# Performance work log

Measured on AMD Instinct MI355X. Metric: run time of the kernel, lower is better.

The kernel has to match this reference:

```python
import jax, jax.numpy as jnp
import numpy as np

D_MODEL, D_STATE, D_CONV, EXPAND = 1024, 16, 4, 2
D_INNER = EXPAND * D_MODEL  # 2048
DT_RANK = (D_MODEL + 15) // 16  # 64
BATCH, SEQ = 2, 2048


def setup_inputs() -> dict:
    key = jax.random.key(0)
    ks = jax.random.split(key, 8)
    s = 0.02
    A = jnp.tile(jnp.arange(1, D_STATE + 1, dtype=jnp.float32), (D_INNER, 1))
    return {
        "x": jax.random.normal(ks[0], (BATCH, SEQ, D_MODEL), jnp.float32),
        "in_proj_w": jax.random.normal(ks[1], (D_MODEL, 2 * D_INNER), jnp.float32) * s,
        "conv_w": jax.random.normal(ks[2], (D_INNER, 1, D_CONV), jnp.float32) * s,
        "conv_b": jnp.zeros((D_INNER,), jnp.float32),
        "x_proj_w": jax.random.normal(ks[3], (D_INNER, DT_RANK + 2 * D_STATE), jnp.float32) * s,
        "dt_proj_w": jax.random.normal(ks[4], (DT_RANK, D_INNER), jnp.float32) * s,
        "dt_proj_b": jnp.zeros((D_INNER,), jnp.float32),
        "A_log": jnp.log(A),
        "D": jnp.ones((D_INNER,), jnp.float32),
        "out_proj_w": jax.random.normal(ks[5], (D_INNER, D_MODEL), jnp.float32) * s,
    }


def _mamba(x, in_proj_w, conv_w, conv_b, x_proj_w, dt_proj_w, dt_proj_b, A_log, D, out_proj_w):
    d_inner, d_state = A_log.shape
    dt_rank = dt_proj_w.shape[0]
    seq_len = x.shape[1]

    xr = x @ in_proj_w                       # (B, L, 2*ED)
    xb, res = jnp.split(xr, 2, axis=-1)      # each (B, L, ED)

    # causal depthwise conv1d (torch pads both sides then truncates to seq_len
    # == left-pad-only causal conv)
    xc = jnp.swapaxes(xb, 1, 2)              # (B, ED, L)
    xc = jax.lax.conv_general_dilated(
        xc, conv_w, window_strides=(1,),
        padding=[(conv_w.shape[-1] - 1, 0)],
        dimension_numbers=("NCH", "OIH", "NCH"),
        feature_group_count=d_inner)
    xc = xc + conv_b[None, :, None]
    u = jax.nn.silu(jnp.swapaxes(xc, 1, 2))  # (B, L, ED)

    dbc = u @ x_proj_w                       # (B, L, dt_rank + 2*N)
    dt, Bc, Cc = jnp.split(dbc, [dt_rank, dt_rank + d_state], axis=-1)
    dt = jax.nn.softplus(dt @ dt_proj_w + dt_proj_b)  # (B, L, ED)
    A = -jnp.exp(A_log)                      # (ED, N)

    def step(h, xs):
        dt_i, B_i, C_i, u_i = xs             # (B,ED), (B,N), (B,N), (B,ED)
        dA = jnp.exp(dt_i[:, :, None] * A)   # (B, ED, N)
        h = h * dA + (dt_i * u_i)[:, :, None] * B_i[:, None, :]
        y = jnp.einsum("bdn,bn->bd", h, C_i) + D * u_i
        return h, y

    h0 = jnp.zeros((x.shape[0], d_inner, d_state), x.dtype)
    xs = (jnp.swapaxes(dt, 0, 1), jnp.swapaxes(Bc, 0, 1),
          jnp.swapaxes(Cc, 0, 1), jnp.swapaxes(u, 0, 1))
    _, ys = jax.lax.scan(step, h0, xs)       # ys: (L, B, ED)
    y_ssm = jnp.swapaxes(ys, 0, 1)           # (B, L, ED)

    y = y_ssm * jax.nn.silu(res)
    return y @ out_proj_w                    # (B, L, d_model)


def reference(x, in_proj_w, conv_w, conv_b, x_proj_w, dt_proj_w, dt_proj_b, A_log, D, out_proj_w):
    return _mamba(x, in_proj_w, conv_w, conv_b, x_proj_w, dt_proj_w, dt_proj_b, A_log, D, out_proj_w)
```

## Files before the change

### kernel.cpp

```cpp
#include <hip/hip_runtime.h>
#include <cstddef>
#include <cstdint>

#define BATCH 2
#define SEQ   2048
#define DM    1024
#define ED    2048
#define NS    16
#define DR    64
#define NROWS (BATCH*SEQ)

#define NCHUNK 32
#define CLEN   64
#define CSTATES (BATCH*ED*NS)

#define OFF_XB    ((size_t)0)
#define OFF_RESH  ((size_t)8388608)
#define OFF_U     ((size_t)12582912)
#define OFF_DT    ((size_t)20971520)
#define OFF_DBC   ((size_t)29360128)
#define OFF_PART  ((size_t)29753344)

typedef _Float16 half8 __attribute__((ext_vector_type(8)));
typedef _Float16 half4 __attribute__((ext_vector_type(4)));
typedef float    floatx4 __attribute__((ext_vector_type(4)));

__device__ __forceinline__ float silu_f(float x) { return x / (1.f + __expf(-x)); }

__device__ __forceinline__ void gload_lds16(const _Float16* g, _Float16* l) {
  __builtin_amdgcn_global_load_lds(
      (const __attribute__((address_space(1))) void*)g,
      (__attribute__((address_space(3))) void*)l, 16, 0, 0);
}

template<int BN, int WGM, int WGN, int EPI, int KSPLIT>
__global__ __launch_bounds__(256)
void hgemm(const _Float16* __restrict__ A, int lda,
           const _Float16* __restrict__ Bt, int ldb,
           float* __restrict__ C, _Float16* __restrict__ Ch,
           size_t cslice, int N, int K) {
  constexpr int BM = 128;
  constexpr int FM = BM / 16 / WGM;
  constexpr int FN = BN / 16 / WGN;
  __shared__ _Float16 sA[BM * 32];
  __shared__ _Float16 sB[BN * 32];
  const int tid = threadIdx.x;
  const int ln  = tid & 63;
  const int wid = tid >> 6;
  const int wm  = wid % WGM;
  const int wn  = wid / WGM;
  const int m0  = blockIdx.y * BM;
  const int n0  = blockIdx.x * BN;
  const int l15 = ln & 15;
  const int q   = ln >> 4;

  const int kLen = K / KSPLIT;
  const int kbeg = blockIdx.z * kLen;
  if (KSPLIT > 1) C += (size_t)blockIdx.z * cslice;

  floatx4 acc[FM][FN];
  #pragma unroll
  for (int i = 0; i < FM; ++i)
    #pragma unroll
    for (int j = 0; j < FN; ++j)
      acc[i][j] = floatx4{0.f, 0.f, 0.f, 0.f};

  for (int k0 = kbeg; k0 < kbeg + kLen; k0 += 32) {
    __syncthreads();
    #pragma unroll
    for (int s = 0; s < (BM * 4 + 255) / 256; ++s) {
      const int i = s * 256 + tid;
      if (BM * 4 % 256 == 0 || i < BM * 4) {
        const int m = i >> 2;
        const int cg = (i & 3) ^ ((m >> 1) & 3);
        gload_lds16(A + (size_t)(m0 + m) * lda + k0 + cg * 8, sA + i * 8);
      }
    }
    #pragma unroll
    for (int s = 0; s < (BN * 4 + 255) / 256; ++s) {
      const int i = s * 256 + tid;
      if (BN * 4 % 256 == 0 || i < BN * 4) {
        const int n = i >> 2;
        const int cg = (i & 3) ^ ((n >> 1) & 3);
        gload_lds16(Bt + (size_t)(n0 + n) * ldb + k0 + cg * 8, sB + i * 8);
      }
    }
    __syncthreads();

    half8 af[FM], bf[FN];
    #pragma unroll
    for (int fm = 0; fm < FM; ++fm) {
      const int mr = wm * FM * 16 + fm * 16 + l15;
      const int cl = q ^ ((mr >> 1) & 3);
      af[fm] = *(const half8*)(sA + mr * 32 + cl * 8);
    }
    #pragma unroll
    for (int fn = 0; fn < FN; ++fn) {
      const int nr = wn * FN * 16 + fn * 16 + l15;
      const int cl = q ^ ((nr >> 1) & 3);
      bf[fn] = *(const half8*)(sB + nr * 32 + cl * 8);
    }
    #pragma unroll
    for (int fm = 0; fm < FM; ++fm)
      #pragma unroll
      for (int fn = 0; fn < FN; ++fn)
        acc[fm][fn] = __builtin_amdgcn_mfma_f32_16x16x32_f16(
            af[fm], bf[fn], acc[fm][fn], 0, 0, 0);
  }

  #pragma unroll
  for (int fm = 0; fm < FM; ++fm) {
    #pragma unroll
    for (int fn = 0; fn < FN; ++fn) {
      const int col = n0 + wn * FN * 16 + fn * 16 + l15;
      #pragma unroll
      for (int r = 0; r < 4; ++r) {
        const int row = m0 + wm * FM * 16 + fm * 16 + q * 4 + r;
        const float v = acc[fm][fn][r];
        if (EPI == 2) {
          if (col < ED) C[(size_t)row * ED + col] = v;
          else          Ch[(size_t)row * ED + (col - ED)] = (_Float16)silu_f(v);
        } else {
          C[(size_t)row * N + col] = v;
        }
      }
    }
  }
}

__global__ __launch_bounds__(256)
void cvt_half_kernel(const float* __restrict__ src, _Float16* __restrict__ dst) {
  const int i = (blockIdx.x * 256 + threadIdx.x) * 4;
  const float4 v = *(const float4*)(src + i);
  half4 o;
  o[0] = (_Float16)v.x; o[1] = (_Float16)v.y;
  o[2] = (_Float16)v.z; o[3] = (_Float16)v.w;
  *(half4*)(dst + i) = o;
}

__global__ __launch_bounds__(256)
void transpose_h_kernel(const float* __restrict__ src, _Float16* __restrict__ dst,
                        int R, int C) {
  __shared__ float t[32][33];
  const int tx = threadIdx.x & 31, ty = threadIdx.x >> 5;
  const int c0 = blockIdx.x * 32, r0 = blockIdx.y * 32;
  #pragma unroll
  for (int s = 0; s < 4; ++s)
    t[ty + s * 8][tx] = src[(size_t)(r0 + ty + s * 8) * C + c0 + tx];
  __syncthreads();
  #pragma unroll
  for (int s = 0; s < 4; ++s)
    dst[(size_t)(c0 + ty + s * 8) * R + r0 + tx] = (_Float16)t[tx][ty + s * 8];
}

template<int EPI>
__global__ __launch_bounds__(256)
void sgemm128(const float* __restrict__ A, int lda,
              const float* __restrict__ Bm, const float* __restrict__ bias,
              float* __restrict__ C, int N, int K) {
  __shared__ float As[8][128];
  __shared__ float Bs[8][128];
  const int tid  = threadIdx.x;
  const int m0   = blockIdx.y * 128;
  const int n0   = blockIdx.x * 128;
  const int tx   = tid & 15;
  const int ty   = tid >> 4;
  const int arow = tid >> 1;
  const int acol = (tid & 1) * 4;
  const int brow = tid >> 5;
  const int bcol = (tid & 31) * 4;

  const float* Ap = A + (size_t)(m0 + arow) * lda + acol;
  const float* Bp = Bm + (size_t)brow * N + n0 + bcol;

  float acc[8][8];
  #pragma unroll
  for (int i = 0; i < 8; ++i)
    #pragma unroll
    for (int j = 0; j < 8; ++j) acc[i][j] = 0.f;

  for (int k0 = 0; k0 < K; k0 += 8) {
    const float4 av = *(const float4*)(Ap + k0);
    const float4 bv = *(const float4*)(Bp + (size_t)k0 * N);
    __syncthreads();
    As[acol + 0][arow] = av.x;
    As[acol + 1][arow] = av.y;
    As[acol + 2][arow] = av.z;
    As[acol + 3][arow] = av.w;
    *(float4*)&Bs[brow][bcol] = bv;
    __syncthreads();
    #pragma unroll
    for (int k = 0; k < 8; ++k) {
      float a[8], b[8];
      *(float4*)(a)     = *(const float4*)&As[k][ty * 8];
      *(float4*)(a + 4) = *(const float4*)&As[k][ty * 8 + 4];
      *(float4*)(b)     = *(const float4*)&Bs[k][tx * 8];
      *(float4*)(b + 4) = *(const float4*)&Bs[k][tx * 8 + 4];
      #pragma unroll
      for (int i = 0; i < 8; ++i)
        #pragma unroll
        for (int j = 0; j < 8; ++j)
          acc[i][j] = fmaf(a[i], b[j], acc[i][j]);
    }
  }

  #pragma unroll
  for (int i = 0; i < 8; ++i) {
    float* Cp = C + (size_t)(m0 + ty * 8 + i) * N + n0 + tx * 8;
    #pragma unroll
    for (int j = 0; j < 8; ++j) {
      float v = acc[i][j];
      if (EPI == 1) {
        v += bias[n0 + tx * 8 + j];
        v = fmaxf(v, 0.f) + log1pf(__expf(-fabsf(v)));
      }
      Cp[j] = v;
    }
  }
}

__global__ __launch_bounds__(256)
void conv_silu_kernel(const float* __restrict__ xb, const float* __restrict__ w,
                      const float* __restrict__ cb, float* __restrict__ u,
                      _Float16* __restrict__ u_h) {
  const int idx = blockIdx.x * 256 + threadIdx.x;
  const int d = idx & (ED - 1);
  const int t = (idx >> 11) & (SEQ - 1);
  const float4 wv = ((const float4*)w)[d];
  const float* base = xb + (size_t)(idx >> 11) * ED + d;
  float acc = cb[d];
  acc = fmaf(wv.w, base[0], acc);
  if (t >= 1) acc = fmaf(wv.z, base[-ED], acc);
  if (t >= 2) acc = fmaf(wv.y, base[-2 * ED], acc);
  if (t >= 3) acc = fmaf(wv.x, base[-3 * ED], acc);
  const float v = silu_f(acc);
  u[idx] = v;
  u_h[idx] = (_Float16)v;
}

__global__ __launch_bounds__(256)
void xproj_reduce(const float* __restrict__ part, float* __restrict__ dbc) {
  const int idx = blockIdx.x * 256 + threadIdx.x;
  float s = 0.f;
  #pragma unroll
  for (int r = 0; r < 8; ++r) s += part[(size_t)r * NROWS * 96 + idx];
  dbc[idx] = s;
}

__global__ __launch_bounds__(256)
void scan2_summary(const float* __restrict__ dt, const float* __restrict__ u,
                   const float* __restrict__ dbc, const float* __restrict__ A_log,
                   float* __restrict__ Pbuf, float* __restrict__ Sbuf) {
  const int d = blockIdx.x * 256 + threadIdx.x;
  const int b = blockIdx.y;
  const int g = blockIdx.z;

  float Adn[16];
  {
    const float4* al = (const float4*)(A_log + (size_t)d * NS);
    #pragma unroll
    for (int i = 0; i < 4; ++i) {
      const float4 v = al[i];
      Adn[i * 4 + 0] = -__expf(v.x); Adn[i * 4 + 1] = -__expf(v.y);
      Adn[i * 4 + 2] = -__expf(v.z); Adn[i * 4 + 3] = -__expf(v.w);
    }
  }
  float P[16], S[16];
  #pragma unroll
  for (int n = 0; n < 16; ++n) { P[n] = 1.f; S[n] = 0.f; }

  const size_t row0 = (size_t)b * SEQ + (size_t)g * CLEN;
  const float* dtp = dt + row0 * ED + d;
  const float* up  = u  + row0 * ED + d;

  for (int t = 0; t < CLEN; ++t) {
    const float dti = dtp[(size_t)t * ED];
    const float ui  = up[(size_t)t * ED];
    const float4* bc = (const float4*)(dbc + (row0 + t) * 96 + DR);
    float Bv[16];
    #pragma unroll
    for (int i = 0; i < 4; ++i) {
      const float4 v = bc[i];
      Bv[i * 4 + 0] = v.x; Bv[i * 4 + 1] = v.y;
      Bv[i * 4 + 2] = v.z; Bv[i * 4 + 3] = v.w;
    }
    const float dtu = dti * ui;
    #pragma unroll
    for (int n = 0; n < 16; ++n) {
      const float a = __expf(dti * Adn[n]);
      S[n] = fmaf(S[n], a, dtu * Bv[n]);
      P[n] *= a;
    }
  }
  const size_t c0 = (size_t)g * CSTATES + ((size_t)(b * ED + d)) * NS;
  #pragma unroll
  for (int i = 0; i < 4; ++i) {
    *(float4*)(Pbuf + c0 + i * 4) = float4{P[i*4], P[i*4+1], P[i*4+2], P[i*4+3]};
    *(float4*)(Sbuf + c0 + i * 4) = float4{S[i*4], S[i*4+1], S[i*4+2], S[i*4+3]};
  }
}

__global__ __launch_bounds__(256)
void scan2_compose(float* __restrict__ Pbuf, const float* __restrict__ Sbuf) {
  const unsigned c = blockIdx.x * 256 + threadIdx.x;
  float h = 0.f;
  for (int g = 0; g < NCHUNK; ++g) {
    const size_t idx = (size_t)g * CSTATES + c;
    const float p = Pbuf[idx], s = Sbuf[idx];
    Pbuf[idx] = h;
    h = fmaf(p, h, s);
  }
}

__global__ __launch_bounds__(256)
void scan2_apply(const float* __restrict__ dt, const float* __restrict__ u,
                 const float* __restrict__ dbc, const float* __restrict__ A_log,
                 const float* __restrict__ Dp, const float* __restrict__ Pbuf,
                 _Float16* __restrict__ resh) {
  const int d = blockIdx.x * 256 + threadIdx.x;
  const int b = blockIdx.y;
  const int g = blockIdx.z;

  float Adn[16];
  {
    const float4* al = (const float4*)(A_log + (size_t)d * NS);
    #pragma unroll
    for (int i = 0; i < 4; ++i) {
      const float4 v = al[i];
      Adn[i * 4 + 0] = -__expf(v.x); Adn[i * 4 + 1] = -__expf(v.y);
      Adn[i * 4 + 2] = -__expf(v.z); Adn[i * 4 + 3] = -__expf(v.w);
    }
  }
  const float Dd = Dp[d];
  float h[16];
  const size_t c0 = (size_t)g * CSTATES + ((size_t)(b * ED + d)) * NS;
  #pragma unroll
  for (int i = 0; i < 4; ++i) {
    const float4 v = *(const float4*)(Pbuf + c0 + i * 4);
    h[i * 4 + 0] = v.x; h[i * 4 + 1] = v.y;
    h[i * 4 + 2] = v.z; h[i * 4 + 3] = v.w;
  }

  const size_t row0 = (size_t)b * SEQ + (size_t)g * CLEN;
  const float* dtp = dt + row0 * ED + d;
  const float* up  = u  + row0 * ED + d;
  _Float16* rp = resh + row0 * ED + d;

  for (int t = 0; t < CLEN; ++t) {
    const float dti = dtp[(size_t)t * ED];
    const float ui  = up[(size_t)t * ED];
    const float4* bc = (const float4*)(dbc + (row0 + t) * 96 + DR);
    float Bv[16], Cv[16];
    #pragma unroll
    for (int i = 0; i < 4; ++i) {
      const float4 v = bc[i];
      Bv[i * 4 + 0] = v.x; Bv[i * 4 + 1] = v.y;
      Bv[i * 4 + 2] = v.z; Bv[i * 4 + 3] = v.w;
      const float4 w = bc[4 + i];
      Cv[i * 4 + 0] = w.x; Cv[i * 4 + 1] = w.y;
      Cv[i * 4 + 2] = w.z; Cv[i * 4 + 3] = w.w;
    }
    const float dtu = dti * ui;
    float y = Dd * ui;
    #pragma unroll
    for (int n = 0; n < 16; ++n) {
      const float a = __expf(dti * Adn[n]);
      h[n] = fmaf(h[n], a, dtu * Bv[n]);
      y = fmaf(h[n], Cv[n], y);
    }
    const float sres = (float)rp[(size_t)t * ED];
    rp[(size_t)t * ED] = (_Float16)(y * sres);
  }
}

extern "C" void kernel_launch(void* const* d_in, const int* in_sizes, int n_in,
                              void* d_out, int out_size, void* d_ws, size_t ws_size,
                              hipStream_t stream) {
  (void)in_sizes; (void)n_in; (void)out_size; (void)ws_size;
  const float* x     = (const float*)d_in[0];
  const float* Win   = (const float*)d_in[1];
  const float* convw = (const float*)d_in[2];
  const float* convb = (const float*)d_in[3];
  const float* Wx    = (const float*)d_in[4];
  const float* Wdt   = (const float*)d_in[5];
  const float* bdt   = (const float*)d_in[6];
  const float* Alog  = (const float*)d_in[7];
  const float* Dp    = (const float*)d_in[8];
  const float* Wout  = (const float*)d_in[9];

  float* ws   = (float*)d_ws;
  float* xb   = ws + OFF_XB;
  _Float16* resh = (_Float16*)(ws + OFF_RESH);
  float* u    = ws + OFF_U;
  float* dt   = ws + OFF_DT;
  float* dbc  = ws + OFF_DBC;
  float* part = ws + OFF_PART;
  float* Pbuf = part;
  float* Sbuf = part + (size_t)NCHUNK * CSTATES;
  _Float16* Woutt = (_Float16*)(part + 4194304);
  _Float16* Wxt   = (_Float16*)(part + 5242880);
  float* out  = (float*)d_out;

  _Float16* x_h  = (_Float16*)(ws + OFF_DT);
  _Float16* Wint = (_Float16*)(ws + OFF_DT + 2097152);
  _Float16* u_h  = (_Float16*)(ws + OFF_DT + 4194304);

  cvt_half_kernel<<<(NROWS * DM) / 1024, 256, 0, stream>>>(x, x_h);
  transpose_h_kernel<<<dim3((2 * ED) / 32, DM / 32), 256, 0, stream>>>(
      Win, Wint, DM, 2 * ED);
  transpose_h_kernel<<<dim3(96 / 32, ED / 32), 256, 0, stream>>>(
      Wx, Wxt, ED, 96);
  transpose_h_kernel<<<dim3(DM / 32, ED / 32), 256, 0, stream>>>(
      Wout, Woutt, ED, DM);
  hgemm<128, 2, 2, 2, 1><<<dim3((2 * ED) / 128, NROWS / 128), 256, 0, stream>>>(
      x_h, DM, Wint, DM, xb, resh, 0, 2 * ED, DM);
  conv_silu_kernel<<<(NROWS * ED) / 256, 256, 0, stream>>>(xb, convw, convb, u, u_h);
  hgemm<96, 4, 1, 0, 8><<<dim3(1, NROWS / 128, 8), 256, 0, stream>>>(
      u_h, ED, Wxt, ED, part, nullptr, (size_t)NROWS * 96, 96, ED);
  xproj_reduce<<<(NROWS * 96) / 256, 256, 0, stream>>>(part, dbc);
  sgemm128<1><<<dim3(ED / 128, NROWS / 128), 256, 0, stream>>>(
      dbc, 96, Wdt, bdt, dt, ED, DR);
  scan2_summary<<<dim3(ED / 256, BATCH, NCHUNK), 256, 0, stream>>>(
      dt, u, dbc, Alog, Pbuf, Sbuf);
  scan2_compose<<<CSTATES / 256, 256, 0, stream>>>(Pbuf, Sbuf);
  scan2_apply<<<dim3(ED / 256, BATCH, NCHUNK), 256, 0, stream>>>(
      dt, u, dbc, Alog, Dp, Pbuf, resh);
  hgemm<64, 4, 1, 0, 1><<<dim3(DM / 64, NROWS / 128), 256, 0, stream>>>(
      resh, ED, Woutt, ED, out, nullptr, 0, DM, ED);
}
```

Measured before the change: 374.6 us.

## Fuse prep kernels, recompute conv in scan, move dt_proj to fp16 MFMA

Merges the input cast and the three weight transposes, plus a new Wdt transpose, into one prep kernel to cut launch count. The scan kernels now recompute the causal conv and SiLU from xb instead of reading a stored fp32 u buffer, which removes that write and reread. dt_proj moves from the fp32 SIMT sgemm to the fp16 MFMA hgemm with a fused bias+softplus epilogue. The scan chunking goes from 32 chunks of 64 to 64 chunks of 32, giving more parallelism but more compose work, and the half-precision dt input adds rounding error.

Result: faster. 364.5 us (-2.7%).

```diff
diff --git a/kernel.cpp b/kernel.cpp
--- a/kernel.cpp
+++ b/kernel.cpp
@@ -10,13 +10,13 @@
 #define DR    64
 #define NROWS (BATCH*SEQ)
 
-#define NCHUNK 32
-#define CLEN   64
+#define NCHUNK 64
+#define CLEN   32
 #define CSTATES (BATCH*ED*NS)
 
 #define OFF_XB    ((size_t)0)
 #define OFF_RESH  ((size_t)8388608)
-#define OFF_U     ((size_t)12582912)
+#define OFF_PS    ((size_t)12582912)
 #define OFF_DT    ((size_t)20971520)
 #define OFF_DBC   ((size_t)29360128)
 #define OFF_PART  ((size_t)29753344)
@@ -37,6 +37,7 @@
 __global__ __launch_bounds__(256)
 void hgemm(const _Float16* __restrict__ A, int lda,
            const _Float16* __restrict__ Bt, int ldb,
+           const float* __restrict__ bias,
            float* __restrict__ C, _Float16* __restrict__ Ch,
            size_t cslice, int N, int K) {
   constexpr int BM = 128;
@@ -116,10 +117,14 @@
       #pragma unroll
       for (int r = 0; r < 4; ++r) {
         const int row = m0 + wm * FM * 16 + fm * 16 + q * 4 + r;
-        const float v = acc[fm][fn][r];
+        float v = acc[fm][fn][r];
         if (EPI == 2) {
           if (col < ED) C[(size_t)row * ED + col] = v;
           else          Ch[(size_t)row * ED + (col - ED)] = (_Float16)silu_f(v);
+        } else if (EPI == 3) {
+          v += bias[col];
+          v = fmaxf(v, 0.f) + log1pf(__expf(-fabsf(v)));
+          C[(size_t)row * N + col] = v;
         } else {
           C[(size_t)row * N + col] = v;
         }
@@ -128,22 +133,13 @@
   }
 }
 
-__global__ __launch_bounds__(256)
-void cvt_half_kernel(const float* __restrict__ src, _Float16* __restrict__ dst) {
-  const int i = (blockIdx.x * 256 + threadIdx.x) * 4;
-  const float4 v = *(const float4*)(src + i);
-  half4 o;
-  o[0] = (_Float16)v.x; o[1] = (_Float16)v.y;
-  o[2] = (_Float16)v.z; o[3] = (_Float16)v.w;
-  *(half4*)(dst + i) = o;
-}
-
-__global__ __launch_bounds__(256)
-void transpose_h_kernel(const float* __restrict__ src, _Float16* __restrict__ dst,
-                        int R, int C) {
+__device__ __forceinline__ void transpose_tile(const float* __restrict__ src,
+                                               _Float16* __restrict__ dst,
+                                               int R, int C, int bx, int by,
+                                               int tid) {
   __shared__ float t[32][33];
-  const int tx = threadIdx.x & 31, ty = threadIdx.x >> 5;
-  const int c0 = blockIdx.x * 32, r0 = blockIdx.y * 32;
+  const int tx = tid & 31, ty = tid >> 5;
+  const int c0 = bx * 32, r0 = by * 32;
   #pragma unroll
   for (int s = 0; s < 4; ++s)
     t[ty + s * 8][tx] = src[(size_t)(r0 + ty + s * 8) * C + c0 + tx];
@@ -153,76 +149,39 @@
     dst[(size_t)(c0 + ty + s * 8) * R + r0 + tx] = (_Float16)t[tx][ty + s * 8];
 }
 
-template<int EPI>
-__global__ __launch_bounds__(256)
-void sgemm128(const float* __restrict__ A, int lda,
-              const float* __restrict__ Bm, const float* __restrict__ bias,
-              float* __restrict__ C, int N, int K) {
-  __shared__ float As[8][128];
-  __shared__ float Bs[8][128];
-  const int tid  = threadIdx.x;
-  const int m0   = blockIdx.y * 128;
-  const int n0   = blockIdx.x * 128;
-  const int tx   = tid & 15;
-  const int ty   = tid >> 4;
-  const int arow = tid >> 1;
-  const int acol = (tid & 1) * 4;
-  const int brow = tid >> 5;
-  const int bcol = (tid & 31) * 4;
-
-  const float* Ap = A + (size_t)(m0 + arow) * lda + acol;
-  const float* Bp = Bm + (size_t)brow * N + n0 + bcol;
-
-  float acc[8][8];
-  #pragma unroll
-  for (int i = 0; i < 8; ++i)
-    #pragma unroll
-    for (int j = 0; j < 8; ++j) acc[i][j] = 0.f;
-
-  for (int k0 = 0; k0 < K; k0 += 8) {
-    const float4 av = *(const float4*)(Ap + k0);
-    const float4 bv = *(const float4*)(Bp + (size_t)k0 * N);
-    __syncthreads();
-    As[acol + 0][arow] = av.x;
-    As[acol + 1][arow] = av.y;
-    As[acol + 2][arow] = av.z;
-    As[acol + 3][arow] = av.w;
-    *(float4*)&Bs[brow][bcol] = bv;
-    __syncthreads();
-    #pragma unroll
-    for (int k = 0; k < 8; ++k) {
-      float a[8], b[8];
-      *(float4*)(a)     = *(const float4*)&As[k][ty * 8];
-      *(float4*)(a + 4) = *(const float4*)&As[k][ty * 8 + 4];
-      *(float4*)(b)     = *(const float4*)&Bs[k][tx * 8];
-      *(float4*)(b + 4) = *(const float4*)&Bs[k][tx * 8 + 4];
-      #pragma unroll
-      for (int i = 0; i < 8; ++i)
-        #pragma unroll
-        for (int j = 0; j < 8; ++j)
-          acc[i][j] = fmaf(a[i], b[j], acc[i][j]);
-    }
-  }
-
-  #pragma unroll
-  for (int i = 0; i < 8; ++i) {
-    float* Cp = C + (size_t)(m0 + ty * 8 + i) * N + n0 + tx * 8;
-    #pragma unroll
-    for (int j = 0; j < 8; ++j) {
-      float v = acc[i][j];
-      if (EPI == 1) {
-        v += bias[n0 + tx * 8 + j];
-        v = fmaxf(v, 0.f) + log1pf(__expf(-fabsf(v)));
-      }
-      Cp[j] = v;
-    }
+#define PREP_BLOCKS 10560
+__global__ __launch_bounds__(256)
+void prep_kernel(const float* __restrict__ x, _Float16* __restrict__ x_h,
+                 const float* __restrict__ Win, _Float16* __restrict__ Wint,
+                 const float* __restrict__ Wout, _Float16* __restrict__ Woutt,
+                 const float* __restrict__ Wx, _Float16* __restrict__ Wxt,
+                 const float* __restrict__ Wdt, _Float16* __restrict__ Wdtt) {
+  const int bid = blockIdx.x, tid = threadIdx.x;
+  if (bid < 4096) {
+    const int i = bid * 1024 + tid * 4;
+    const float4 v = *(const float4*)(x + i);
+    half4 o;
+    o[0] = (_Float16)v.x; o[1] = (_Float16)v.y;
+    o[2] = (_Float16)v.z; o[3] = (_Float16)v.w;
+    *(half4*)(x_h + i) = o;
+  } else if (bid < 8192) {
+    const int t = bid - 4096;
+    transpose_tile(Win, Wint, DM, 2 * ED, t & 127, t >> 7, tid);
+  } else if (bid < 10240) {
+    const int t = bid - 8192;
+    transpose_tile(Wout, Woutt, ED, DM, t & 31, t >> 5, tid);
+  } else if (bid < 10432) {
+    const int t = bid - 10240;
+    transpose_tile(Wx, Wxt, ED, 96, t % 3, t / 3, tid);
+  } else {
+    const int t = bid - 10432;
+    transpose_tile(Wdt, Wdtt, DR, ED, t & 63, t >> 6, tid);
   }
 }
 
 __global__ __launch_bounds__(256)
 void conv_silu_kernel(const float* __restrict__ xb, const float* __restrict__ w,
-                      const float* __restrict__ cb, float* __restrict__ u,
-                      _Float16* __restrict__ u_h) {
+                      const float* __restrict__ cb, _Float16* __restrict__ u_h) {
   const int idx = blockIdx.x * 256 + threadIdx.x;
   const int d = idx & (ED - 1);
   const int t = (idx >> 11) & (SEQ - 1);
@@ -233,22 +192,31 @@
   if (t >= 1) acc = fmaf(wv.z, base[-ED], acc);
   if (t >= 2) acc = fmaf(wv.y, base[-2 * ED], acc);
   if (t >= 3) acc = fmaf(wv.x, base[-3 * ED], acc);
-  const float v = silu_f(acc);
-  u[idx] = v;
-  u_h[idx] = (_Float16)v;
-}
-
-__global__ __launch_bounds__(256)
-void xproj_reduce(const float* __restrict__ part, float* __restrict__ dbc) {
+  u_h[idx] = (_Float16)silu_f(acc);
+}
+
+__global__ __launch_bounds__(256)
+void xproj_reduce(const float* __restrict__ part, float* __restrict__ dbc,
+                  _Float16* __restrict__ dbc64h) {
   const int idx = blockIdx.x * 256 + threadIdx.x;
   float s = 0.f;
   #pragma unroll
   for (int r = 0; r < 8; ++r) s += part[(size_t)r * NROWS * 96 + idx];
   dbc[idx] = s;
-}
-
-__global__ __launch_bounds__(256)
-void scan2_summary(const float* __restrict__ dt, const float* __restrict__ u,
+  const int col = idx % 96;
+  if (col < DR) dbc64h[(idx / 96) * DR + col] = (_Float16)s;
+}
+
+__device__ __forceinline__ void conv_init(const float* xbp, int tg0,
+                                          float& x1, float& x2, float& x3) {
+  x1 = (tg0 >= 1) ? xbp[-(int)ED] : 0.f;
+  x2 = (tg0 >= 2) ? xbp[-2 * (int)ED] : 0.f;
+  x3 = (tg0 >= 3) ? xbp[-3 * (int)ED] : 0.f;
+}
+
+__global__ __launch_bounds__(256)
+void scan2_summary(const float* __restrict__ dt, const float* __restrict__ xb,
+                   const float* __restrict__ convw, const float* __restrict__ convb,
                    const float* __restrict__ dbc, const float* __restrict__ A_log,
                    float* __restrict__ Pbuf, float* __restrict__ Sbuf) {
   const int d = blockIdx.x * 256 + threadIdx.x;
@@ -265,17 +233,31 @@
       Adn[i * 4 + 2] = -__expf(v.z); Adn[i * 4 + 3] = -__expf(v.w);
     }
   }
+  const float4 wv = ((const float4*)convw)[d];
+  const float cbd = convb[d];
+
   float P[16], S[16];
   #pragma unroll
   for (int n = 0; n < 16; ++n) { P[n] = 1.f; S[n] = 0.f; }
 
-  const size_t row0 = (size_t)b * SEQ + (size_t)g * CLEN;
+  const int tg0 = g * CLEN;
+  const size_t row0 = (size_t)b * SEQ + tg0;
   const float* dtp = dt + row0 * ED + d;
-  const float* up  = u  + row0 * ED + d;
+  const float* xbp = xb + row0 * ED + d;
+  float x1, x2, x3;
+  conv_init(xbp, tg0, x1, x2, x3);
 
   for (int t = 0; t < CLEN; ++t) {
+    const float xt  = xbp[(size_t)t * ED];
     const float dti = dtp[(size_t)t * ED];
-    const float ui  = up[(size_t)t * ED];
+    float cv = cbd;
+    cv = fmaf(wv.w, xt, cv);
+    cv = fmaf(wv.z, x1, cv);
+    cv = fmaf(wv.y, x2, cv);
+    cv = fmaf(wv.x, x3, cv);
+    const float ui = silu_f(cv);
+    x3 = x2; x2 = x1; x1 = xt;
+
     const float4* bc = (const float4*)(dbc + (row0 + t) * 96 + DR);
     float Bv[16];
     #pragma unroll
@@ -313,7 +295,8 @@
 }
 
 __global__ __launch_bounds__(256)
-void scan2_apply(const float* __restrict__ dt, const float* __restrict__ u,
+void scan2_apply(const float* __restrict__ dt, const float* __restrict__ xb,
+                 const float* __restrict__ convw, const float* __restrict__ convb,
                  const float* __restrict__ dbc, const float* __restrict__ A_log,
                  const float* __restrict__ Dp, const float* __restrict__ Pbuf,
                  _Float16* __restrict__ resh) {
@@ -331,7 +314,10 @@
       Adn[i * 4 + 2] = -__expf(v.z); Adn[i * 4 + 3] = -__expf(v.w);
     }
   }
+  const float4 wv = ((const float4*)convw)[d];
+  const float cbd = convb[d];
   const float Dd = Dp[d];
+
   float h[16];
   const size_t c0 = (size_t)g * CSTATES + ((size_t)(b * ED + d)) * NS;
   #pragma unroll
@@ -341,14 +327,25 @@
     h[i * 4 + 2] = v.z; h[i * 4 + 3] = v.w;
   }
 
-  const size_t row0 = (size_t)b * SEQ + (size_t)g * CLEN;
+  const int tg0 = g * CLEN;
+  const size_t row0 = (size_t)b * SEQ + tg0;
   const float* dtp = dt + row0 * ED + d;
-  const float* up  = u  + row0 * ED + d;
+  const float* xbp = xb + row0 * ED + d;
   _Float16* rp = resh + row0 * ED + d;
+  float x1, x2, x3;
+  conv_init(xbp, tg0, x1, x2, x3);
 
   for (int t = 0; t < CLEN; ++t) {
+    const float xt  = xbp[(size_t)t * ED];
     const float dti = dtp[(size_t)t * ED];
-    const float ui  = up[(size_t)t * ED];
+    float cv = cbd;
+    cv = fmaf(wv.w, xt, cv);
+    cv = fmaf(wv.z, x1, cv);
+    cv = fmaf(wv.y, x2, cv);
+    cv = fmaf(wv.x, x3, cv);
+    const float ui = silu_f(cv);
+    x3 = x2; x2 = x1; x1 = xt;
+
     const float4* bc = (const float4*)(dbc + (row0 + t) * 96 + DR);
     float Bv[16], Cv[16];
     #pragma unroll
@@ -391,40 +388,36 @@
   float* ws   = (float*)d_ws;
   float* xb   = ws + OFF_XB;
   _Float16* resh = (_Float16*)(ws + OFF_RESH);
-  float* u    = ws + OFF_U;
+  float* Pbuf = ws + OFF_PS;
+  float* Sbuf = ws + OFF_PS + 4194304;
   float* dt   = ws + OFF_DT;
   float* dbc  = ws + OFF_DBC;
   float* part = ws + OFF_PART;
-  float* Pbuf = part;
-  float* Sbuf = part + (size_t)NCHUNK * CSTATES;
-  _Float16* Woutt = (_Float16*)(part + 4194304);
-  _Float16* Wxt   = (_Float16*)(part + 5242880);
+  _Float16* Woutt  = (_Float16*)(part + 4194304);
+  _Float16* Wxt    = (_Float16*)(part + 5242880);
+  _Float16* dbc64h = (_Float16*)(part + 5341184);
+  _Float16* Wdtt   = (_Float16*)(part + 5472256);
   float* out  = (float*)d_out;
 
   _Float16* x_h  = (_Float16*)(ws + OFF_DT);
   _Float16* Wint = (_Float16*)(ws + OFF_DT + 2097152);
   _Float16* u_h  = (_Float16*)(ws + OFF_DT + 4194304);
 
-  cvt_half_kernel<<<(NROWS * DM) / 1024, 256, 0, stream>>>(x, x_h);
-  transpose_h_kernel<<<dim3((2 * ED) / 32, DM / 32), 256, 0, stream>>>(
-      Win, Wint, DM, 2 * ED);
-  transpose_h_kernel<<<dim3(96 / 32, ED / 32), 256, 0, stream>>>(
-      Wx, Wxt, ED, 96);
-  transpose_h_kernel<<<dim3(DM / 32, ED / 32), 256, 0, stream>>>(
-      Wout, Woutt, ED, DM);
+  prep_kernel<<<PREP_BLOCKS, 256, 0, stream>>>(
+      x, x_h, Win, Wint, Wout, Woutt, Wx, Wxt, Wdt, Wdtt);
   hgemm<128, 2, 2, 2, 1><<<dim3((2 * ED) / 128, NROWS / 128), 256, 0, stream>>>(
-      x_h, DM, Wint, DM, xb, resh, 0, 2 * ED, DM);
-  conv_silu_kernel<<<(NROWS * ED) / 256, 256, 0, stream>>>(xb, convw, convb, u, u_h);
+      x_h, DM, Wint, DM, nullptr, xb, resh, 0, 2 * ED, DM);
+  conv_silu_kernel<<<(NROWS * ED) / 256, 256, 0, stream>>>(xb, convw, convb, u_h);
   hgemm<96, 4, 1, 0, 8><<<dim3(1, NROWS / 128, 8), 256, 0, stream>>>(
-      u_h, ED, Wxt, ED, part, nullptr, (size_t)NROWS * 96, 96, ED);
-  xproj_reduce<<<(NROWS * 96) / 256, 256, 0, stream>>>(part, dbc);
-  sgemm128<1><<<dim3(ED / 128, NROWS / 128), 256, 0, stream>>>(
-      dbc, 96, Wdt, bdt, dt, ED, DR);
+      u_h, ED, Wxt, ED, nullptr, part, nullptr, (size_t)NROWS * 96, 96, ED);
+  xproj_reduce<<<(NROWS * 96) / 256, 256, 0, stream>>>(part, dbc, dbc64h);
+  hgemm<128, 2, 2, 3, 1><<<dim3(ED / 128, NROWS / 128), 256, 0, stream>>>(
+      dbc64h, DR, Wdtt, DR, bdt, dt, nullptr, 0, ED, DR);
   scan2_summary<<<dim3(ED / 256, BATCH, NCHUNK), 256, 0, stream>>>(
-      dt, u, dbc, Alog, Pbuf, Sbuf);
+      dt, xb, convw, convb, dbc, Alog, Pbuf, Sbuf);
   scan2_compose<<<CSTATES / 256, 256, 0, stream>>>(Pbuf, Sbuf);
   scan2_apply<<<dim3(ED / 256, BATCH, NCHUNK), 256, 0, stream>>>(
-      dt, u, dbc, Alog, Dp, Pbuf, resh);
+      dt, xb, convw, convb, dbc, Alog, Dp, Pbuf, resh);
   hgemm<64, 4, 1, 0, 1><<<dim3(DM / 64, NROWS / 128), 256, 0, stream>>>(
-      resh, ED, Woutt, ED, out, nullptr, 0, DM, ED);
-}
+      resh, ED, Woutt, ED, nullptr, out, nullptr, 0, DM, ED);
+}
```
